# Optimization experiments

Hardware: AMD Instinct MI355X
Metric: run time of the kernel (lower is better)

The kernel has to match this reference:

```python
import jax, jax.numpy as jnp
import numpy as np

N, E = 30000, 600000
D_NODE, E_DIM, H1, H2, D_OUT = 128, 128, 256, 128, 128


def setup_inputs() -> dict:
    key = jax.random.key(0)
    ks = jax.random.split(key, 24)
    w = lambda k, shape: jax.random.normal(k, shape, jnp.float32) * 0.05
    return {
        "node_feat": jax.random.normal(ks[0], (N, D_NODE), jnp.float32),
        "src": jax.random.randint(ks[1], (E,), 0, N, jnp.int32),
        "dst": jax.random.randint(ks[2], (E,), 0, N, jnp.int32),
        "W_e1": w(ks[3], (2 * D_NODE + E_DIM, H1)), "b_e1": w(ks[4], (H1,)),
        "W_e2": w(ks[5], (H1, E_DIM)), "b_e2": w(ks[6], (E_DIM,)),
        "W_n1": w(ks[7], (D_NODE + E_DIM, H1)), "b_n1": w(ks[8], (H1,)),
        "W_n2": w(ks[9], (H1, H2)), "b_n2": w(ks[10], (H2,)),
        "W_el1": w(ks[11], (2 * H2, H1)), "b_el1": w(ks[12], (H1,)),
        "W_el2": w(ks[13], (H1, E_DIM)), "b_el2": w(ks[14], (E_DIM,)),
        "W_logit": w(ks[15], (E_DIM, 2)), "b_logit": w(ks[16], (2,)),
        "W_nro": w(ks[17], (H2, D_OUT)), "b_nro": w(ks[18], (D_OUT,)),
        "W_ero": w(ks[19], (E_DIM, D_OUT)), "b_ero": w(ks[20], (D_OUT,)),
        "msg_passing_steps": 2,
    }


def reference(node_feat, src, dst,
              W_e1, b_e1, W_e2, b_e2,
              W_n1, b_n1, W_n2, b_n2,
              W_el1, b_el1, W_el2, b_el2,
              W_logit, b_logit, W_nro, b_nro, W_ero, b_ero,
              msg_passing_steps):
    n_nodes = node_feat.shape[0]
    edge_dim = W_e2.shape[1]
    # incoming messages 'h', initialized to zeros
    h = jnp.zeros((n_nodes, edge_dim), node_feat.dtype)
    for _ in range(msg_passing_steps):
        # apply_edges: edge_feat = fc_edge2(relu(fc_edge([h_src, nf_src, nf_dst])))
        inp = jnp.concatenate([h[src], node_feat[src], node_feat[dst]], axis=-1)  # [E, edge_dim+2*D]
        edge_feat = jax.nn.relu(inp @ W_e1 + b_e1) @ W_e2 + b_e2                   # [E, edge_dim]
        # update_all with fn.sum: scatter-sum messages into destination nodes
        h = jax.ops.segment_sum(edge_feat, dst, num_segments=n_nodes)
    # apply_nodes: node_feat <- fc_node2(relu(fc_node([node_feat, h])))
    nf = jax.nn.relu(jnp.concatenate([node_feat, h], axis=-1) @ W_n1 + b_n1) @ W_n2 + b_n2  # [N, H2]
    n_out = nf @ W_nro + b_nro
    # compute_edge_logits: symmetric edge MLP over updated node reps
    s, d = nf[src], nf[dst]
    edge_mlp = lambda x: jax.nn.relu(x @ W_el1 + b_el1) @ W_el2 + b_el2
    comb = edge_mlp(jnp.concatenate([s, d], axis=-1)) + edge_mlp(jnp.concatenate([d, s], axis=-1))
    e_out_readout = comb @ W_ero + b_ero
    e_out = comb @ W_logit + b_logit
    return n_out, e_out_readout, e_out
```

## Files before the change

kernel.cpp:

```cpp
#include <hip/hip_runtime.h>
#include <hip/hip_bf16.h>

typedef __bf16 bf16;
typedef unsigned short u16;
typedef bf16 bf16x8 __attribute__((ext_vector_type(8)));
typedef bf16 bf16x4 __attribute__((ext_vector_type(4)));
typedef float f32x4 __attribute__((ext_vector_type(4)));

constexpr int NN = 30000;
constexpr int NE = 600000;
constexpr int D  = 128;

__device__ inline f32x4 mfma16(bf16x8 a, bf16x8 b, f32x4 c) {
    return __builtin_amdgcn_mfma_f32_16x16x32_bf16(a, b, c, 0, 0, 0);
}
__device__ inline bf16x8 ld8(const bf16* p) {
    return *reinterpret_cast<const bf16x8*>(p);
}
__device__ inline bf16x8 cvt8(const float* p) {
    float4 v0 = reinterpret_cast<const float4*>(p)[0];
    float4 v1 = reinterpret_cast<const float4*>(p)[1];
    bf16x8 r;
    r[0] = (bf16)v0.x; r[1] = (bf16)v0.y; r[2] = (bf16)v0.z; r[3] = (bf16)v0.w;
    r[4] = (bf16)v1.x; r[5] = (bf16)v1.y; r[6] = (bf16)v1.z; r[7] = (bf16)v1.w;
    return r;
}
__device__ inline int swz512(int row, int byteInRow) {
    return row * 512 + (byteInRow ^ ((row & 15) << 4));
}

struct TMat { const float* src; bf16* dst; int K; int Nc; };
struct TPack { TMat m[12]; };

__global__ void transpose_cast_kernel(TPack p) {
    TMat mm = p.m[blockIdx.x];
    int total = mm.K * mm.Nc;
    for (int idx = blockIdx.y * blockDim.x + threadIdx.x; idx < total;
         idx += gridDim.y * blockDim.x) {
        int c = idx / mm.K;
        int k = idx - c * mm.K;
        mm.dst[idx] = (bf16)mm.src[k * mm.Nc + c];
    }
}

__global__ void fuse_kernel(const float* __restrict__ W_el2,
                            const float* __restrict__ W_ero,
                            const float* __restrict__ W_logit,
                            const float* __restrict__ b_el2,
                            const float* __restrict__ b_ero,
                            const float* __restrict__ b_logit,
                            bf16* __restrict__ W2eroT, bf16* __restrict__ W2lgT,
                            float* __restrict__ b2ero, float* __restrict__ b2lg) {
    int k = blockIdx.x;
    int c = threadIdx.x;
    if (c >= 144) return;
    if (k < 256) {
        if (c < 128) {
            float s = 0.f;
            for (int j = 0; j < 128; ++j) s += W_el2[k * 128 + j] * W_ero[j * 128 + c];
            W2eroT[c * 256 + k] = (bf16)s;
        } else {
            int cc = c - 128;
            float s = 0.f;
            if (cc < 2) for (int j = 0; j < 128; ++j) s += W_el2[k * 128 + j] * W_logit[j * 2 + cc];
            W2lgT[cc * 256 + k] = (bf16)s;
        }
    } else {
        if (c < 128) {
            float s = b_ero[c];
            for (int j = 0; j < 128; ++j) s += 2.f * b_el2[j] * W_ero[j * 128 + c];
            b2ero[c] = s;
        } else if (c < 130) {
            int cc = c - 128;
            float s = b_logit[cc];
            for (int j = 0; j < 128; ++j) s += 2.f * b_el2[j] * W_logit[j * 2 + cc];
            b2lg[cc] = s;
        }
    }
}

__global__ void hist_kernel(const int* __restrict__ dst, int* __restrict__ counts) {
    int e = blockIdx.x * blockDim.x + threadIdx.x;
    if (e < NE) atomicAdd(counts + dst[e], 1);
}

__global__ void scan_kernel(const int* __restrict__ counts, int* __restrict__ offsets,
                            int* __restrict__ cursor) {
    __shared__ int part[1024];
    const int t = threadIdx.x;
    const int base = t * 30;
    int local[30];
    int s = 0;
#pragma unroll
    for (int i = 0; i < 30; ++i) {
        int idx = base + i;
        int v = (idx < NN) ? counts[idx] : 0;
        local[i] = s;
        s += v;
    }
    part[t] = s;
    __syncthreads();
    for (int off = 1; off < 1024; off <<= 1) {
        int x = (t >= off) ? part[t - off] : 0;
        __syncthreads();
        part[t] += x;
        __syncthreads();
    }
    int chunkExcl = (t == 0) ? 0 : part[t - 1];
#pragma unroll
    for (int i = 0; i < 30; ++i) {
        int idx = base + i;
        if (idx < NN) {
            int excl = chunkExcl + local[i];
            offsets[idx] = excl;
            cursor[idx] = excl;
        }
    }
    if (t == 0) offsets[NN] = NE;
}

__global__ void scatter_kernel(const int* __restrict__ src, const int* __restrict__ dst,
                               int* __restrict__ cursor, int* __restrict__ perm,
                               u16* __restrict__ srcS, u16* __restrict__ dstS) {
    int e = blockIdx.x * blockDim.x + threadIdx.x;
    if (e < NE) {
        int d = dst[e];
        int p = atomicAdd(cursor + d, 1);
        perm[p] = e;
        srcS[p] = (u16)src[e];
        dstS[p] = (u16)d;
    }
}

template<bool IN_BF16>
__global__ void __launch_bounds__(256, 4)
node_pre_kernel(const float* __restrict__ inF, const bf16* __restrict__ inB,
                const bf16* __restrict__ WT,
                const float* __restrict__ bias0,
                bf16* __restrict__ O1, bf16* __restrict__ O2) {
    const int half = blockIdx.y;
    const int r0 = blockIdx.x * 64;
    const int t = threadIdx.x, wv = t >> 6, l = t & 63, lr = l & 15, qk = l >> 4;
    int row[4];
#pragma unroll
    for (int m = 0; m < 4; ++m) { int r = r0 + m * 16 + lr; row[m] = r < NN ? r : NN - 1; }
    int coln[4];
#pragma unroll
    for (int n = 0; n < 4; ++n) coln[n] = wv * 64 + n * 16 + lr;
    f32x4 acc[4][4];
#pragma unroll
    for (int m = 0; m < 4; ++m)
#pragma unroll
        for (int n = 0; n < 4; ++n) acc[m][n] = 0.f;
#pragma unroll
    for (int ks = 0; ks < 4; ++ks) {
        const int kg = ks * 32 + qk * 8;
        bf16x8 a[4], b[4];
#pragma unroll
        for (int m = 0; m < 4; ++m)
            a[m] = IN_BF16 ? ld8(inB + row[m] * D + kg) : cvt8(inF + row[m] * D + kg);
#pragma unroll
        for (int n = 0; n < 4; ++n) b[n] = ld8(WT + (half * 256 + coln[n]) * 128 + kg);
#pragma unroll
        for (int m = 0; m < 4; ++m)
#pragma unroll
            for (int n = 0; n < 4; ++n) acc[m][n] = mfma16(a[m], b[n], acc[m][n]);
    }
    bf16* O = half ? O2 : O1;
#pragma unroll
    for (int n = 0; n < 4; ++n) {
        float bia = (half == 0 && bias0) ? bias0[coln[n]] : 0.f;
#pragma unroll
        for (int m = 0; m < 4; ++m)
#pragma unroll
            for (int j = 0; j < 4; ++j) {
                int gr = r0 + m * 16 + qk * 4 + j;
                if (gr < NN) O[gr * 256 + coln[n]] = (bf16)(acc[m][n][j] + bia);
            }
    }
}

template<bool HBF>
__global__ void __launch_bounds__(256, 4)
s2_update_kernel(const void* __restrict__ h1, const bf16* __restrict__ WtopT,
                 bf16* __restrict__ S) {
    const int r0 = blockIdx.x * 64;
    const int t = threadIdx.x, wv = t >> 6, l = t & 63, lr = l & 15, qk = l >> 4;
    int row[4];
#pragma unroll
    for (int m = 0; m < 4; ++m) { int r = r0 + m * 16 + lr; row[m] = r < NN ? r : NN - 1; }
    int coln[4];
#pragma unroll
    for (int n = 0; n < 4; ++n) coln[n] = wv * 64 + n * 16 + lr;
    f32x4 acc[4][4];
#pragma unroll
    for (int m = 0; m < 4; ++m)
#pragma unroll
        for (int n = 0; n < 4; ++n) acc[m][n] = 0.f;
#pragma unroll
    for (int ks = 0; ks < 4; ++ks) {
        const int kg = ks * 32 + qk * 8;
        bf16x8 a[4], b[4];
#pragma unroll
        for (int m = 0; m < 4; ++m) {
            if constexpr (HBF) a[m] = ld8((const bf16*)h1 + row[m] * D + kg);
            else               a[m] = cvt8((const float*)h1 + row[m] * D + kg);
        }
#pragma unroll
        for (int n = 0; n < 4; ++n) b[n] = ld8(WtopT + coln[n] * 128 + kg);
#pragma unroll
        for (int m = 0; m < 4; ++m)
#pragma unroll
            for (int n = 0; n < 4; ++n) acc[m][n] = mfma16(a[m], b[n], acc[m][n]);
    }
#pragma unroll
    for (int n = 0; n < 4; ++n)
#pragma unroll
        for (int m = 0; m < 4; ++m)
#pragma unroll
            for (int j = 0; j < 4; ++j) {
                int gr = r0 + m * 16 + qk * 4 + j;
                if (gr < NN) {
                    int idx = gr * 256 + coln[n];
                    S[idx] = (bf16)((float)S[idx] + acc[m][n][j]);
                }
            }
}

__global__ void __launch_bounds__(256, 8)
seg_sum_kernel(const bf16* __restrict__ S, const bf16* __restrict__ Bm,
               const int* __restrict__ offsets, const u16* __restrict__ srcS,
               bf16* __restrict__ T) {
    const int gw = (blockIdx.x * blockDim.x + threadIdx.x) >> 6;
    if (gw >= NN) return;
    const int l = threadIdx.x & 63;
    const int beg = offsets[gw], end = offsets[gw + 1];
    bf16x4 bv = *reinterpret_cast<const bf16x4*>(Bm + (size_t)gw * 256 + l * 4);
    const float b0 = (float)bv[0], b1 = (float)bv[1], b2 = (float)bv[2], b3 = (float)bv[3];
    float t0 = 0.f, t1 = 0.f, t2 = 0.f, t3 = 0.f;
    int i = beg;
    for (; i + 4 <= end; i += 4) {
        int s0 = srcS[i], s1 = srcS[i + 1], s2 = srcS[i + 2], s3 = srcS[i + 3];
        bf16x4 a0 = *reinterpret_cast<const bf16x4*>(S + (size_t)s0 * 256 + l * 4);
        bf16x4 a1 = *reinterpret_cast<const bf16x4*>(S + (size_t)s1 * 256 + l * 4);
        bf16x4 a2 = *reinterpret_cast<const bf16x4*>(S + (size_t)s2 * 256 + l * 4);
        bf16x4 a3 = *reinterpret_cast<const bf16x4*>(S + (size_t)s3 * 256 + l * 4);
        float v;
        v = (float)a0[0] + b0; t0 += v > 0.f ? v : 0.f;
        v = (float)a0[1] + b1; t1 += v > 0.f ? v : 0.f;
        v = (float)a0[2] + b2; t2 += v > 0.f ? v : 0.f;
        v = (float)a0[3] + b3; t3 += v > 0.f ? v : 0.f;
        v = (float)a1[0] + b0; t0 += v > 0.f ? v : 0.f;
        v = (float)a1[1] + b1; t1 += v > 0.f ? v : 0.f;
        v = (float)a1[2] + b2; t2 += v > 0.f ? v : 0.f;
        v = (float)a1[3] + b3; t3 += v > 0.f ? v : 0.f;
        v = (float)a2[0] + b0; t0 += v > 0.f ? v : 0.f;
        v = (float)a2[1] + b1; t1 += v > 0.f ? v : 0.f;
        v = (float)a2[2] + b2; t2 += v > 0.f ? v : 0.f;
        v = (float)a2[3] + b3; t3 += v > 0.f ? v : 0.f;
        v = (float)a3[0] + b0; t0 += v > 0.f ? v : 0.f;
        v = (float)a3[1] + b1; t1 += v > 0.f ? v : 0.f;
        v = (float)a3[2] + b2; t2 += v > 0.f ? v : 0.f;
        v = (float)a3[3] + b3; t3 += v > 0.f ? v : 0.f;
    }
    for (; i < end; ++i) {
        int s0 = srcS[i];
        bf16x4 a0 = *reinterpret_cast<const bf16x4*>(S + (size_t)s0 * 256 + l * 4);
        float v;
        v = (float)a0[0] + b0; t0 += v > 0.f ? v : 0.f;
        v = (float)a0[1] + b1; t1 += v > 0.f ? v : 0.f;
        v = (float)a0[2] + b2; t2 += v > 0.f ? v : 0.f;
        v = (float)a0[3] + b3; t3 += v > 0.f ? v : 0.f;
    }
    bf16x4 o;
    o[0] = (bf16)t0; o[1] = (bf16)t1; o[2] = (bf16)t2; o[3] = (bf16)t3;
    *reinterpret_cast<bf16x4*>(T + (size_t)gw * 256 + l * 4) = o;
}

__global__ void __launch_bounds__(256, 4)
h_gemm_kernel(const bf16* __restrict__ T, const bf16* __restrict__ We2T,
              const float* __restrict__ b_e2, const int* __restrict__ deg,
              bf16* __restrict__ h) {
    const int r0 = blockIdx.x * 64;
    const int t = threadIdx.x, wv = t >> 6, l = t & 63, lr = l & 15, qk = l >> 4;
    int row[4];
#pragma unroll
    for (int m = 0; m < 4; ++m) { int r = r0 + m * 16 + lr; row[m] = r < NN ? r : NN - 1; }
    int col2[2];
#pragma unroll
    for (int n = 0; n < 2; ++n) col2[n] = wv * 32 + n * 16 + lr;
    f32x4 acc[4][2];
#pragma unroll
    for (int m = 0; m < 4; ++m)
#pragma unroll
        for (int n = 0; n < 2; ++n) acc[m][n] = 0.f;
#pragma unroll
    for (int ks = 0; ks < 8; ++ks) {
        const int kg = ks * 32 + qk * 8;
        bf16x8 a[4], b[2];
#pragma unroll
        for (int m = 0; m < 4; ++m) a[m] = ld8(T + (size_t)row[m] * 256 + kg);
#pragma unroll
        for (int n = 0; n < 2; ++n) b[n] = ld8(We2T + col2[n] * 256 + kg);
#pragma unroll
        for (int m = 0; m < 4; ++m)
#pragma unroll
            for (int n = 0; n < 2; ++n) acc[m][n] = mfma16(a[m], b[n], acc[m][n]);
    }
#pragma unroll
    for (int n = 0; n < 2; ++n) {
        float bw = b_e2[col2[n]];
#pragma unroll
        for (int m = 0; m < 4; ++m)
#pragma unroll
            for (int j = 0; j < 4; ++j) {
                int gr = r0 + m * 16 + qk * 4 + j;
                if (gr < NN)
                    h[(size_t)gr * D + col2[n]] = (bf16)(acc[m][n][j] + (float)deg[gr] * bw);
            }
    }
}

template<bool HBF>
__global__ void __launch_bounds__(256, 2)
node_mlp_kernel(const float* __restrict__ node_feat,
                const void* __restrict__ h2,
                const bf16* __restrict__ Wn1T,
                const bf16* __restrict__ Wn2T,
                const float* __restrict__ b_n1,
                const float* __restrict__ b_n2,
                bf16* __restrict__ nf2_bf) {
    __shared__ __align__(16) char sH[64 * 512];
    const int t = threadIdx.x, wv = t >> 6, l = t & 63, lr = l & 15, qk = l >> 4;
    const int r0 = blockIdx.x * 64;
    int row[4];
#pragma unroll
    for (int m = 0; m < 4; ++m) { int r = r0 + m * 16 + lr; row[m] = r < NN ? r : NN - 1; }
    int coln[4];
#pragma unroll
    for (int n = 0; n < 4; ++n) coln[n] = wv * 64 + n * 16 + lr;
    f32x4 acc[4][4];
#pragma unroll
    for (int m = 0; m < 4; ++m)
#pragma unroll
        for (int n = 0; n < 4; ++n) acc[m][n] = 0.f;
#pragma unroll
    for (int ks = 0; ks < 4; ++ks) {
        const int kg = ks * 32 + qk * 8;
        bf16x8 a[4], b[4];
#pragma unroll
        for (int m = 0; m < 4; ++m) a[m] = cvt8(node_feat + (size_t)row[m] * D + kg);
#pragma unroll
        for (int n = 0; n < 4; ++n) b[n] = ld8(Wn1T + coln[n] * 256 + kg);
#pragma unroll
        for (int m = 0; m < 4; ++m)
#pragma unroll
            for (int n = 0; n < 4; ++n) acc[m][n] = mfma16(a[m], b[n], acc[m][n]);
#pragma unroll
        for (int m = 0; m < 4; ++m) {
            if constexpr (HBF) a[m] = ld8((const bf16*)h2 + (size_t)row[m] * D + kg);
            else               a[m] = cvt8((const float*)h2 + (size_t)row[m] * D + kg);
        }
#pragma unroll
        for (int n = 0; n < 4; ++n) b[n] = ld8(Wn1T + coln[n] * 256 + 128 + kg);
#pragma unroll
        for (int m = 0; m < 4; ++m)
#pragma unroll
            for (int n = 0; n < 4; ++n) acc[m][n] = mfma16(a[m], b[n], acc[m][n]);
    }
#pragma unroll
    for (int n = 0; n < 4; ++n) {
        float bia = b_n1[coln[n]];
#pragma unroll
        for (int m = 0; m < 4; ++m)
#pragma unroll
            for (int j = 0; j < 4; ++j) {
                int r = m * 16 + qk * 4 + j;
                float v = acc[m][n][j] + bia;
                v = v > 0.f ? v : 0.f;
                *reinterpret_cast<bf16*>(sH + swz512(r, coln[n] * 2)) = (bf16)v;
            }
    }
    __syncthreads();
    int col2[2];
#pragma unroll
    for (int n = 0; n < 2; ++n) col2[n] = wv * 32 + n * 16 + lr;
    f32x4 acc2[4][2];
#pragma unroll
    for (int m = 0; m < 4; ++m)
#pragma unroll
        for (int n = 0; n < 2; ++n) acc2[m][n] = 0.f;
#pragma unroll
    for (int ks = 0; ks < 8; ++ks) {
        const int k0 = ks * 32 + qk * 8;
        bf16x8 a[4], b[2];
#pragma unroll
        for (int m = 0; m < 4; ++m)
            a[m] = *reinterpret_cast<const bf16x8*>(sH + swz512(m * 16 + lr, k0 * 2));
#pragma unroll
        for (int n = 0; n < 2; ++n) b[n] = ld8(Wn2T + col2[n] * 256 + k0);
#pragma unroll
        for (int m = 0; m < 4; ++m)
#pragma unroll
            for (int n = 0; n < 2; ++n) acc2[m][n] = mfma16(a[m], b[n], acc2[m][n]);
    }
#pragma unroll
    for (int n = 0; n < 2; ++n) {
        float bia = b_n2[col2[n]];
#pragma unroll
        for (int m = 0; m < 4; ++m)
#pragma unroll
            for (int j = 0; j < 4; ++j) {
                int gr = r0 + m * 16 + qk * 4 + j;
                if (gr < NN) nf2_bf[(size_t)gr * D + col2[n]] = (bf16)(acc2[m][n][j] + bia);
            }
    }
}

__global__ void __launch_bounds__(256, 4)
edge_logit_sorted(const bf16* __restrict__ U, const bf16* __restrict__ V,
                  const int* __restrict__ perm, const u16* __restrict__ srcS,
                  const u16* __restrict__ dstS,
                  const bf16* __restrict__ W2eroT, const bf16* __restrict__ W2lgT,
                  const float* __restrict__ b2ero, const float* __restrict__ b2lg,
                  float* __restrict__ e_ro, float* __restrict__ e_lg) {
    __shared__ int s_e[128];
    __shared__ int s_s[128];
    __shared__ int s_d[128];
    const int t = threadIdx.x, wv = t >> 6, l = t & 63, lr = l & 15, qk = l >> 4;
    const int bid = (int)blockIdx.x;
    const int cpx = (int)(gridDim.x >> 3);
    const int sbid = (bid & 7) * cpx + (bid >> 3);
    const int p0 = sbid * 128;
    if (t < 128) {
        int p = min(p0 + t, NE - 1);
        s_e[t] = perm[p];
        s_s[t] = (int)srcS[p];
        s_d[t] = (int)dstS[p];
    }
    __syncthreads();

    int is[2], id[2];
#pragma unroll
    for (int m = 0; m < 2; ++m) {
        int el = wv * 32 + m * 16 + lr;
        is[m] = s_s[el];
        id[m] = s_d[el];
    }
    f32x4 aro[2][8];
    f32x4 alg[2];
#pragma unroll
    for (int m = 0; m < 2; ++m) {
        alg[m] = 0.f;
#pragma unroll
        for (int n = 0; n < 8; ++n) aro[m][n] = 0.f;
    }
#pragma unroll
    for (int ks = 0; ks < 8; ++ks) {
        const int kg = ks * 32 + qk * 8;
        bf16x8 a[2];
#pragma unroll
        for (int m = 0; m < 2; ++m) {
            bf16x8 us = ld8(U + (size_t)is[m] * 256 + kg);
            bf16x8 vd = ld8(V + (size_t)id[m] * 256 + kg);
            bf16x8 ud = ld8(U + (size_t)id[m] * 256 + kg);
            bf16x8 vs = ld8(V + (size_t)is[m] * 256 + kg);
#pragma unroll
            for (int i = 0; i < 8; ++i) {
                float f1 = (float)us[i] + (float)vd[i]; f1 = f1 > 0.f ? f1 : 0.f;
                float f2 = (float)ud[i] + (float)vs[i]; f2 = f2 > 0.f ? f2 : 0.f;
                a[m][i] = (bf16)(f1 + f2);
            }
        }
#pragma unroll
        for (int n = 0; n < 8; ++n) {
            bf16x8 b = ld8(W2eroT + (n * 16 + lr) * 256 + kg);
#pragma unroll
            for (int m = 0; m < 2; ++m) aro[m][n] = mfma16(a[m], b, aro[m][n]);
        }
        bf16x8 blg = ld8(W2lgT + lr * 256 + kg);
#pragma unroll
        for (int m = 0; m < 2; ++m) alg[m] = mfma16(a[m], blg, alg[m]);
    }
#pragma unroll
    for (int n = 0; n < 8; ++n) {
        int col = n * 16 + lr;
        float bia = b2ero[col];
#pragma unroll
        for (int m = 0; m < 2; ++m)
#pragma unroll
            for (int j = 0; j < 4; ++j) {
                int el = wv * 32 + m * 16 + qk * 4 + j;
                e_ro[(size_t)s_e[el] * D + col] = aro[m][n][j] + bia;
            }
    }
    if (lr < 2) {
        float bia = b2lg[lr];
#pragma unroll
        for (int m = 0; m < 2; ++m)
#pragma unroll
            for (int j = 0; j < 4; ++j) {
                int el = wv * 32 + m * 16 + qk * 4 + j;
                e_lg[(size_t)s_e[el] * 2 + lr] = alg[m][j] + bia;
            }
    }
}

__global__ void __launch_bounds__(256, 4)
edge_msg_kernel(const bf16* __restrict__ S, const bf16* __restrict__ Bm,
                const int* __restrict__ src, const int* __restrict__ dst,
                const bf16* __restrict__ We2T,
                const float* __restrict__ b_e2,
                float* __restrict__ h_out) {
    __shared__ int s_src[128];
    __shared__ int s_dst[128];
    const int t = threadIdx.x, wv = t >> 6, l = t & 63, lr = l & 15, qk = l >> 4;
    const int e0 = blockIdx.x * 128;
    if (t < 128)      s_src[t] = src[min(e0 + t, NE - 1)];
    else              s_dst[t - 128] = dst[min(e0 + t - 128, NE - 1)];
    __syncthreads();
    const bf16* pS[2];
    const bf16* pB[2];
#pragma unroll
    for (int m = 0; m < 2; ++m) {
        int el = wv * 32 + m * 16 + lr;
        pS[m] = S + s_src[el] * 256;
        pB[m] = Bm + s_dst[el] * 256;
    }
    f32x4 acc[2][8];
#pragma unroll
    for (int m = 0; m < 2; ++m)
#pragma unroll
        for (int n = 0; n < 8; ++n) acc[m][n] = 0.f;
#pragma unroll
    for (int ks = 0; ks < 8; ++ks) {
        const int kg = ks * 32 + qk * 8;
        bf16x8 a[2];
#pragma unroll
        for (int m = 0; m < 2; ++m) {
            bf16x8 sa = ld8(pS[m] + kg);
            bf16x8 sb = ld8(pB[m] + kg);
#pragma unroll
            for (int i = 0; i < 8; ++i) {
                float f = (float)sa[i] + (float)sb[i];
                a[m][i] = (bf16)(f > 0.f ? f : 0.f);
            }
        }
#pragma unroll
        for (int n = 0; n < 8; ++n) {
            bf16x8 b = ld8(We2T + (n * 16 + lr) * 256 + kg);
#pragma unroll
            for (int m = 0; m < 2; ++m) acc[m][n] = mfma16(a[m], b, acc[m][n]);
        }
    }
#pragma unroll
    for (int n = 0; n < 8; ++n) {
        int col = n * 16 + lr;
        float bia = b_e2[col];
#pragma unroll
        for (int m = 0; m < 2; ++m)
#pragma unroll
            for (int j = 0; j < 4; ++j) {
                int el = wv * 32 + m * 16 + qk * 4 + j;
                if (e0 + el < NE)
                    atomicAdd(h_out + s_dst[el] * D + col, acc[m][n][j] + bia);
            }
    }
}

__global__ void __launch_bounds__(256, 4)
edge_logit_fast(const bf16* __restrict__ U, const bf16* __restrict__ V,
                const int* __restrict__ src, const int* __restrict__ dst,
                const bf16* __restrict__ W2eroT,
                const bf16* __restrict__ W2lgT,
                const float* __restrict__ b2ero, const float* __restrict__ b2lg,
                float* __restrict__ e_ro, float* __restrict__ e_lg) {
    __shared__ int s_src[128];
    __shared__ int s_dst[128];
    const int t = threadIdx.x, wv = t >> 6, l = t & 63, lr = l & 15, qk = l >> 4;
    const int e0 = blockIdx.x * 128;
    if (t < 128)      s_src[t] = src[min(e0 + t, NE - 1)];
    else              s_dst[t - 128] = dst[min(e0 + t - 128, NE - 1)];
    __syncthreads();
    int is[2], id[2];
#pragma unroll
    for (int m = 0; m < 2; ++m) {
        int el = wv * 32 + m * 16 + lr;
        is[m] = s_src[el];
        id[m] = s_dst[el];
    }
    f32x4 aro[2][8];
    f32x4 alg[2];
#pragma unroll
    for (int m = 0; m < 2; ++m) {
        alg[m] = 0.f;
#pragma unroll
        for (int n = 0; n < 8; ++n) aro[m][n] = 0.f;
    }
#pragma unroll
    for (int ks = 0; ks < 8; ++ks) {
        const int kg = ks * 32 + qk * 8;
        bf16x8 a[2];
#pragma unroll
        for (int m = 0; m < 2; ++m) {
            bf16x8 us = ld8(U + is[m] * 256 + kg);
            bf16x8 vd = ld8(V + id[m] * 256 + kg);
            bf16x8 ud = ld8(U + id[m] * 256 + kg);
            bf16x8 vs = ld8(V + is[m] * 256 + kg);
#pragma unroll
            for (int i = 0; i < 8; ++i) {
                float f1 = (float)us[i] + (float)vd[i]; f1 = f1 > 0.f ? f1 : 0.f;
                float f2 = (float)ud[i] + (float)vs[i]; f2 = f2 > 0.f ? f2 : 0.f;
                a[m][i] = (bf16)(f1 + f2);
            }
        }
#pragma unroll
        for (int n = 0; n < 8; ++n) {
            bf16x8 b = ld8(W2eroT + (n * 16 + lr) * 256 + kg);
#pragma unroll
            for (int m = 0; m < 2; ++m) aro[m][n] = mfma16(a[m], b, aro[m][n]);
        }
        bf16x8 blg = ld8(W2lgT + lr * 256 + kg);
#pragma unroll
        for (int m = 0; m < 2; ++m) alg[m] = mfma16(a[m], blg, alg[m]);
    }
#pragma unroll
    for (int n = 0; n < 8; ++n) {
        int col = n * 16 + lr;
        float bia = b2ero[col];
#pragma unroll
        for (int m = 0; m < 2; ++m)
#pragma unroll
            for (int j = 0; j < 4; ++j) {
                int el = wv * 32 + m * 16 + qk * 4 + j;
                int e = e0 + el;
                if (e < NE) e_ro[e * D + col] = aro[m][n][j] + bia;
            }
    }
    if (lr < 2) {
        float bia = b2lg[lr];
#pragma unroll
        for (int m = 0; m < 2; ++m)
#pragma unroll
            for (int j = 0; j < 4; ++j) {
                int el = wv * 32 + m * 16 + qk * 4 + j;
                int e = e0 + el;
                if (e < NE) e_lg[e * 2 + lr] = alg[m][j] + bia;
            }
    }
}

__global__ void __launch_bounds__(256, 4)
nro_kernel(const bf16* __restrict__ nf2_bf, const bf16* __restrict__ WnroT,
           const float* __restrict__ b_nro, float* __restrict__ n_out) {
    const int r0 = blockIdx.x * 64;
    const int t = threadIdx.x, wv = t >> 6, l = t & 63, lr = l & 15, qk = l >> 4;
    int row[4];
#pragma unroll
    for (int m = 0; m < 4; ++m) { int r = r0 + m * 16 + lr; row[m] = r < NN ? r : NN - 1; }
    int col2[2];
#pragma unroll
    for (int n = 0; n < 2; ++n) col2[n] = wv * 32 + n * 16 + lr;
    f32x4 acc[4][2];
#pragma unroll
    for (int m = 0; m < 4; ++m)
#pragma unroll
        for (int n = 0; n < 2; ++n) acc[m][n] = 0.f;
#pragma unroll
    for (int ks = 0; ks < 4; ++ks) {
        const int kg = ks * 32 + qk * 8;
        bf16x8 a[4], b[2];
#pragma unroll
        for (int m = 0; m < 4; ++m) a[m] = ld8(nf2_bf + (size_t)row[m] * D + kg);
#pragma unroll
        for (int n = 0; n < 2; ++n) b[n] = ld8(WnroT + col2[n] * 128 + kg);
#pragma unroll
        for (int m = 0; m < 4; ++m)
#pragma unroll
            for (int n = 0; n < 2; ++n) acc[m][n] = mfma16(a[m], b[n], acc[m][n]);
    }
#pragma unroll
    for (int n = 0; n < 2; ++n) {
        float bia = b_nro[col2[n]];
#pragma unroll
        for (int m = 0; m < 4; ++m)
#pragma unroll
            for (int j = 0; j < 4; ++j) {
                int gr = r0 + m * 16 + qk * 4 + j;
                if (gr < NN) n_out[(size_t)gr * D + col2[n]] = acc[m][n][j] + bia;
            }
    }
}

extern "C" void kernel_launch(void* const* d_in, const int* in_sizes, int n_in,
                              void* d_out, int out_size, void* d_ws, size_t ws_size,
                              hipStream_t stream) {
    const float* node_feat = (const float*)d_in[0];
    const int*   src   = (const int*)d_in[1];
    const int*   dst   = (const int*)d_in[2];
    const float* W_e1  = (const float*)d_in[3];
    const float* b_e1  = (const float*)d_in[4];
    const float* W_e2  = (const float*)d_in[5];
    const float* b_e2  = (const float*)d_in[6];
    const float* W_n1  = (const float*)d_in[7];
    const float* b_n1  = (const float*)d_in[8];
    const float* W_n2  = (const float*)d_in[9];
    const float* b_n2  = (const float*)d_in[10];
    const float* W_el1 = (const float*)d_in[11];
    const float* b_el1 = (const float*)d_in[12];
    const float* W_el2 = (const float*)d_in[13];
    const float* b_el2 = (const float*)d_in[14];
    const float* W_logit = (const float*)d_in[15];
    const float* b_logit = (const float*)d_in[16];
    const float* W_nro = (const float*)d_in[17];
    const float* b_nro = (const float*)d_in[18];
    const float* W_ero = (const float*)d_in[19];
    const float* b_ero = (const float*)d_in[20];

    char* ws = (char*)d_ws;
    bf16* wb = (bf16*)ws;
    bf16* WmbT   = wb;
    bf16* WtopT  = wb + 65536;
    bf16* We2T   = wb + 98304;
    bf16* Wn1T   = wb + 131072;
    bf16* Wn2T   = wb + 196608;
    bf16* WuvT   = wb + 229376;
    bf16* WnroT  = wb + 294912;
    bf16* W2eroT = wb + 311296;
    bf16* W2lgT  = wb + 344064;
    float* fb    = (float*)(ws + 928000);
    float* b2ero = fb;
    float* b2lg  = fb + 128;

    float* out   = (float*)d_out;
    float* n_out = out;
    float* e_ro  = out + 3840000;
    float* e_lg  = out + 80640000;

    TPack pk;
    pk.m[0]  = {W_e1 + 128 * 256, WmbT,              128, 256};
    pk.m[1]  = {W_e1 + 256 * 256, WmbT + 256 * 128,  128, 256};
    pk.m[2]  = {W_e1,             WtopT,             128, 256};
    pk.m[3]  = {W_e2,             We2T,              256, 128};
    pk.m[4]  = {W_n1,             Wn1T,              256, 256};
    pk.m[5]  = {W_n2,             Wn2T,              256, 128};
    pk.m[6]  = {W_el1,            WuvT,              128, 256};
    pk.m[7]  = {W_el1 + 128 * 256, WuvT + 256 * 128, 128, 256};
    pk.m[8]  = {W_nro,            WnroT,             128, 128};
    pk.m[9]  = {W_nro,            WnroT,             128, 128};
    pk.m[10] = {W_nro,            WnroT,             128, 128};
    pk.m[11] = {W_nro,            WnroT,             128, 128};

    const size_t NEED_NEW = 28888576;

    if (ws_size >= NEED_NEW) {
        char* eb = (char*)e_ro;
        bf16* S    = (bf16*)(eb);
        bf16* Bm   = (bf16*)(eb + 15360000);
        bf16* T    = (bf16*)(eb + 30720000);
        bf16* h1   = (bf16*)(eb + 46080000);
        bf16* h2   = (bf16*)(eb + 53760000);
        int* counts  = (int*)(eb + 61440000);
        int* offsets = (int*)(eb + 61560000);
        int* cursor  = (int*)(eb + 61680004);
        bf16* U    = (bf16*)n_out;
        bf16* nf2_bf = (bf16*)(ws + 1048576);
        bf16* Vbuf   = (bf16*)(ws + 8728576);
        int*  perm   = (int*)(ws + 24088576);
        u16*  srcS   = (u16*)(ws + 26488576);
        u16*  dstS   = (u16*)(ws + 27688576);

        transpose_cast_kernel<<<dim3(12, 40), 256, 0, stream>>>(pk);
        fuse_kernel<<<257, 160, 0, stream>>>(W_el2, W_ero, W_logit, b_el2, b_ero, b_logit,
                                             W2eroT, W2lgT, b2ero, b2lg);
        hipMemsetAsync(counts, 0, NN * 4, stream);
        hist_kernel<<<(NE + 255) / 256, 256, 0, stream>>>(dst, counts);
        scan_kernel<<<1, 1024, 0, stream>>>(counts, offsets, cursor);
        scatter_kernel<<<(NE + 255) / 256, 256, 0, stream>>>(src, dst, cursor,
                                                             perm, srcS, dstS);
        node_pre_kernel<false><<<dim3(469, 2), 256, 0, stream>>>(
            node_feat, nullptr, WmbT, b_e1, S, Bm);
        seg_sum_kernel<<<7500, 256, 0, stream>>>(S, Bm, offsets, srcS, T);
        h_gemm_kernel<<<469, 256, 0, stream>>>(T, We2T, b_e2, counts, h1);
        s2_update_kernel<true><<<469, 256, 0, stream>>>(h1, WtopT, S);
        seg_sum_kernel<<<7500, 256, 0, stream>>>(S, Bm, offsets, srcS, T);
        h_gemm_kernel<<<469, 256, 0, stream>>>(T, We2T, b_e2, counts, h2);
        node_mlp_kernel<true><<<469, 256, 0, stream>>>(
            node_feat, h2, Wn1T, Wn2T, b_n1, b_n2, nf2_bf);
        node_pre_kernel<true><<<dim3(469, 2), 256, 0, stream>>>(
            nullptr, nf2_bf, WuvT, b_el1, U, Vbuf);
        edge_logit_sorted<<<4688, 256, 0, stream>>>(
            U, Vbuf, perm, srcS, dstS, W2eroT, W2lgT, b2ero, b2lg, e_ro, e_lg);
        nro_kernel<<<469, 256, 0, stream>>>(nf2_bf, WnroT, b_nro, n_out);
    } else {
        bf16* nf2_bf = (bf16*)(ws + 1048576);
        bf16* Vbuf   = (bf16*)(ws + 9000000);
        float* h1f = n_out;
        bf16*  S   = (bf16*)e_ro;
        bf16*  Bm  = (bf16*)((char*)e_ro + 15360000);
        float* h2f = (float*)((char*)e_ro + 30720000);
        bf16*  U   = (bf16*)n_out;

        transpose_cast_kernel<<<dim3(12, 40), 256, 0, stream>>>(pk);
        fuse_kernel<<<257, 160, 0, stream>>>(W_el2, W_ero, W_logit, b_el2, b_ero, b_logit,
                                             W2eroT, W2lgT, b2ero, b2lg);
        hipMemsetAsync(h1f, 0, (size_t)NN * D * 4, stream);
        hipMemsetAsync(h2f, 0, (size_t)NN * D * 4, stream);
        node_pre_kernel<false><<<dim3(469, 2), 256, 0, stream>>>(
            node_feat, nullptr, WmbT, b_e1, S, Bm);
        edge_msg_kernel<<<4688, 256, 0, stream>>>(S, Bm, src, dst, We2T, b_e2, h1f);
        s2_update_kernel<false><<<469, 256, 0, stream>>>(h1f, WtopT, S);
        edge_msg_kernel<<<4688, 256, 0, stream>>>(S, Bm, src, dst, We2T, b_e2, h2f);
        node_mlp_kernel<false><<<469, 256, 0, stream>>>(
            node_feat, h2f, Wn1T, Wn2T, b_n1, b_n2, nf2_bf);
        node_pre_kernel<true><<<dim3(469, 2), 256, 0, stream>>>(
            nullptr, nf2_bf, WuvT, b_el1, U, Vbuf);
        edge_logit_fast<<<4688, 256, 0, stream>>>(
            U, Vbuf, src, dst, W2eroT, W2lgT, b2ero, b2lg, e_ro, e_lg);
        nro_kernel<<<469, 256, 0, stream>>>(nf2_bf, WnroT, b_nro, n_out);
    }
}
```

Measured before the change: 754.2 us.

## Fold W_e2 into downstream weights to eliminate h GEMM kernels

Precomputes the products W_e2·W_e1(top) and W_e2·W_n1(bottom), plus their bias terms, so the per-node h = T·W_e2 + deg·b_e2 intermediate is never formed. The s2 update and the node MLP now consume the segment-summed T directly with a K=256 GEMM, which removes two h_gemm launches and the h1/h2 round trips through memory. The e_ro output stores are also made nontemporal. In exchange the fused GEMMs do more MFMA work (K 256 instead of 128), add a small weight-fusion kernel, and round the pre-multiplied weights to bf16, which changes numerics slightly.

Result: faster. 735.7 us (-2.5%).

```diff
diff --git a/kernel.cpp b/kernel.cpp
--- a/kernel.cpp
+++ b/kernel.cpp
@@ -79,6 +79,35 @@
     }
 }
 
+__global__ void fuse2_kernel(const float* __restrict__ W_e2,
+                             const float* __restrict__ W_e1,
+                             const float* __restrict__ W_n1,
+                             const float* __restrict__ b_e2,
+                             bf16* __restrict__ WcsT, bf16* __restrict__ WcnT,
+                             float* __restrict__ bcs, float* __restrict__ bcn) {
+    int k = blockIdx.x;
+    int c = threadIdx.x;
+    if (k < 256) {
+        float s1 = 0.f, s2 = 0.f;
+        for (int j = 0; j < 128; ++j) {
+            float w = W_e2[k * 128 + j];
+            s1 += w * W_e1[j * 256 + c];
+            s2 += w * W_n1[(128 + j) * 256 + c];
+        }
+        WcsT[c * 256 + k] = (bf16)s1;
+        WcnT[c * 256 + k] = (bf16)s2;
+    } else {
+        float s1 = 0.f, s2 = 0.f;
+        for (int j = 0; j < 128; ++j) {
+            float b = b_e2[j];
+            s1 += b * W_e1[j * 256 + c];
+            s2 += b * W_n1[(128 + j) * 256 + c];
+        }
+        bcs[c] = s1;
+        bcn[c] = s2;
+    }
+}
+
 __global__ void hist_kernel(const int* __restrict__ dst, int* __restrict__ counts) {
     int e = blockIdx.x * blockDim.x + threadIdx.x;
     if (e < NE) atomicAdd(counts + dst[e], 1);
@@ -180,9 +209,54 @@
     }
 }
 
-template<bool HBF>
 __global__ void __launch_bounds__(256, 4)
-s2_update_kernel(const void* __restrict__ h1, const bf16* __restrict__ WtopT,
+s2_fused_kernel(const bf16* __restrict__ T, const bf16* __restrict__ WcsT,
+                const float* __restrict__ bcs, const int* __restrict__ deg,
+                bf16* __restrict__ S) {
+    const int r0 = blockIdx.x * 64;
+    const int t = threadIdx.x, wv = t >> 6, l = t & 63, lr = l & 15, qk = l >> 4;
+    int row[4];
+#pragma unroll
+    for (int m = 0; m < 4; ++m) { int r = r0 + m * 16 + lr; row[m] = r < NN ? r : NN - 1; }
+    int coln[4];
+#pragma unroll
+    for (int n = 0; n < 4; ++n) coln[n] = wv * 64 + n * 16 + lr;
+    f32x4 acc[4][4];
+#pragma unroll
+    for (int m = 0; m < 4; ++m)
+#pragma unroll
+        for (int n = 0; n < 4; ++n) acc[m][n] = 0.f;
+#pragma unroll
+    for (int ks = 0; ks < 8; ++ks) {
+        const int kg = ks * 32 + qk * 8;
+        bf16x8 a[4], b[4];
+#pragma unroll
+        for (int m = 0; m < 4; ++m) a[m] = ld8(T + (size_t)row[m] * 256 + kg);
+#pragma unroll
+        for (int n = 0; n < 4; ++n) b[n] = ld8(WcsT + coln[n] * 256 + kg);
+#pragma unroll
+        for (int m = 0; m < 4; ++m)
+#pragma unroll
+            for (int n = 0; n < 4; ++n) acc[m][n] = mfma16(a[m], b[n], acc[m][n]);
+    }
+#pragma unroll
+    for (int n = 0; n < 4; ++n) {
+        float bw = bcs[coln[n]];
+#pragma unroll
+        for (int m = 0; m < 4; ++m)
+#pragma unroll
+            for (int j = 0; j < 4; ++j) {
+                int gr = r0 + m * 16 + qk * 4 + j;
+                if (gr < NN) {
+                    int idx = gr * 256 + coln[n];
+                    S[idx] = (bf16)((float)S[idx] + acc[m][n][j] + (float)deg[gr] * bw);
+                }
+            }
+    }
+}
+
+__global__ void __launch_bounds__(256, 4)
+s2_update_kernel(const float* __restrict__ h1, const bf16* __restrict__ WtopT,
                  bf16* __restrict__ S) {
     const int r0 = blockIdx.x * 64;
     const int t = threadIdx.x, wv = t >> 6, l = t & 63, lr = l & 15, qk = l >> 4;
@@ -202,10 +276,7 @@
         const int kg = ks * 32 + qk * 8;
         bf16x8 a[4], b[4];
 #pragma unroll
-        for (int m = 0; m < 4; ++m) {
-            if constexpr (HBF) a[m] = ld8((const bf16*)h1 + row[m] * D + kg);
-            else               a[m] = cvt8((const float*)h1 + row[m] * D + kg);
-        }
+        for (int m = 0; m < 4; ++m) a[m] = cvt8(h1 + (size_t)row[m] * D + kg);
 #pragma unroll
         for (int n = 0; n < 4; ++n) b[n] = ld8(WtopT + coln[n] * 128 + kg);
 #pragma unroll
@@ -277,54 +348,112 @@
     *reinterpret_cast<bf16x4*>(T + (size_t)gw * 256 + l * 4) = o;
 }
 
-__global__ void __launch_bounds__(256, 4)
-h_gemm_kernel(const bf16* __restrict__ T, const bf16* __restrict__ We2T,
-              const float* __restrict__ b_e2, const int* __restrict__ deg,
-              bf16* __restrict__ h) {
+__global__ void __launch_bounds__(256, 2)
+node_mlp_fused(const float* __restrict__ node_feat,
+               const bf16* __restrict__ T2,
+               const bf16* __restrict__ Wn1T,
+               const bf16* __restrict__ WcnT,
+               const bf16* __restrict__ Wn2T,
+               const float* __restrict__ b_n1,
+               const float* __restrict__ bcn,
+               const int* __restrict__ deg,
+               const float* __restrict__ b_n2,
+               bf16* __restrict__ nf2_bf) {
+    __shared__ __align__(16) char sH[64 * 512];
+    const int t = threadIdx.x, wv = t >> 6, l = t & 63, lr = l & 15, qk = l >> 4;
     const int r0 = blockIdx.x * 64;
-    const int t = threadIdx.x, wv = t >> 6, l = t & 63, lr = l & 15, qk = l >> 4;
     int row[4];
 #pragma unroll
     for (int m = 0; m < 4; ++m) { int r = r0 + m * 16 + lr; row[m] = r < NN ? r : NN - 1; }
+    int coln[4];
+#pragma unroll
+    for (int n = 0; n < 4; ++n) coln[n] = wv * 64 + n * 16 + lr;
+    f32x4 acc[4][4];
+#pragma unroll
+    for (int m = 0; m < 4; ++m)
+#pragma unroll
+        for (int n = 0; n < 4; ++n) acc[m][n] = 0.f;
+#pragma unroll
+    for (int ks = 0; ks < 4; ++ks) {
+        const int kg = ks * 32 + qk * 8;
+        bf16x8 a[4], b[4];
+#pragma unroll
+        for (int m = 0; m < 4; ++m) a[m] = cvt8(node_feat + (size_t)row[m] * D + kg);
+#pragma unroll
+        for (int n = 0; n < 4; ++n) b[n] = ld8(Wn1T + coln[n] * 256 + kg);
+#pragma unroll
+        for (int m = 0; m < 4; ++m)
+#pragma unroll
+            for (int n = 0; n < 4; ++n) acc[m][n] = mfma16(a[m], b[n], acc[m][n]);
+    }
+#pragma unroll
+    for (int ks = 0; ks < 8; ++ks) {
+        const int kg = ks * 32 + qk * 8;
+        bf16x8 a[4], b[4];
+#pragma unroll
+        for (int m = 0; m < 4; ++m) a[m] = ld8(T2 + (size_t)row[m] * 256 + kg);
+#pragma unroll
+        for (int n = 0; n < 4; ++n) b[n] = ld8(WcnT + coln[n] * 256 + kg);
+#pragma unroll
+        for (int m = 0; m < 4; ++m)
+#pragma unroll
+            for (int n = 0; n < 4; ++n) acc[m][n] = mfma16(a[m], b[n], acc[m][n]);
+    }
+#pragma unroll
+    for (int n = 0; n < 4; ++n) {
+        float bia = b_n1[coln[n]];
+        float bw  = bcn[coln[n]];
+#pragma unroll
+        for (int m = 0; m < 4; ++m)
+#pragma unroll
+            for (int j = 0; j < 4; ++j) {
+                int r = m * 16 + qk * 4 + j;
+                int gr = r0 + r;
+                float dg = (gr < NN) ? (float)deg[gr] : 0.f;
+                float v = acc[m][n][j] + bia + dg * bw;
+                v = v > 0.f ? v : 0.f;
+                *reinterpret_cast<bf16*>(sH + swz512(r, coln[n] * 2)) = (bf16)v;
+            }
+    }
+    __syncthreads();
     int col2[2];
 #pragma unroll
     for (int n = 0; n < 2; ++n) col2[n] = wv * 32 + n * 16 + lr;
-    f32x4 acc[4][2];
+    f32x4 acc2[4][2];
 #pragma unroll
     for (int m = 0; m < 4; ++m)
 #pragma unroll
-        for (int n = 0; n < 2; ++n) acc[m][n] = 0.f;
+        for (int n = 0; n < 2; ++n) acc2[m][n] = 0.f;
 #pragma unroll
     for (int ks = 0; ks < 8; ++ks) {
-        const int kg = ks * 32 + qk * 8;
+        const int k0 = ks * 32 + qk * 8;
         bf16x8 a[4], b[2];
 #pragma unroll
-        for (int m = 0; m < 4; ++m) a[m] = ld8(T + (size_t)row[m] * 256 + kg);
-#pragma unroll
-        for (int n = 0; n < 2; ++n) b[n] = ld8(We2T + col2[n] * 256 + kg);
-#pragma unroll
-        for (int m = 0; m < 4; ++m)
-#pragma unroll
-            for (int n = 0; n < 2; ++n) acc[m][n] = mfma16(a[m], b[n], acc[m][n]);
+        for (int m = 0; m < 4; ++m)
+            a[m] = *reinterpret_cast<const bf16x8*>(sH + swz512(m * 16 + lr, k0 * 2));
+#pragma unroll
+        for (int n = 0; n < 2; ++n) b[n] = ld8(Wn2T + col2[n] * 256 + k0);
+#pragma unroll
+        for (int m = 0; m < 4; ++m)
+#pragma unroll
+            for (int n = 0; n < 2; ++n) acc2[m][n] = mfma16(a[m], b[n], acc2[m][n]);
     }
 #pragma unroll
     for (int n = 0; n < 2; ++n) {
-        float bw = b_e2[col2[n]];
+        float bia = b_n2[col2[n]];
 #pragma unroll
         for (int m = 0; m < 4; ++m)
 #pragma unroll
             for (int j = 0; j < 4; ++j) {
                 int gr = r0 + m * 16 + qk * 4 + j;
-                if (gr < NN)
-                    h[(size_t)gr * D + col2[n]] = (bf16)(acc[m][n][j] + (float)deg[gr] * bw);
-            }
-    }
-}
-
-template<bool HBF>
+                if (gr < NN) nf2_bf[(size_t)gr * D + col2[n]] = (bf16)(acc2[m][n][j] + bia);
+            }
+    }
+}
+
 __global__ void __launch_bounds__(256, 2)
 node_mlp_kernel(const float* __restrict__ node_feat,
-                const void* __restrict__ h2,
+                const float* __restrict__ h2,
                 const bf16* __restrict__ Wn1T,
                 const bf16* __restrict__ Wn2T,
                 const float* __restrict__ b_n1,
@@ -357,10 +486,7 @@
 #pragma unroll
             for (int n = 0; n < 4; ++n) acc[m][n] = mfma16(a[m], b[n], acc[m][n]);
 #pragma unroll
-        for (int m = 0; m < 4; ++m) {
-            if constexpr (HBF) a[m] = ld8((const bf16*)h2 + (size_t)row[m] * D + kg);
-            else               a[m] = cvt8((const float*)h2 + (size_t)row[m] * D + kg);
-        }
+        for (int m = 0; m < 4; ++m) a[m] = cvt8(h2 + (size_t)row[m] * D + kg);
 #pragma unroll
         for (int n = 0; n < 4; ++n) b[n] = ld8(Wn1T + coln[n] * 256 + 128 + kg);
 #pragma unroll
@@ -413,6 +539,50 @@
             for (int j = 0; j < 4; ++j) {
                 int gr = r0 + m * 16 + qk * 4 + j;
                 if (gr < NN) nf2_bf[(size_t)gr * D + col2[n]] = (bf16)(acc2[m][n][j] + bia);
+            }
+    }
+}
+
+__global__ void __launch_bounds__(256, 4)
+h_gemm_kernel(const bf16* __restrict__ T, const bf16* __restrict__ We2T,
+              const float* __restrict__ b_e2, const int* __restrict__ deg,
+              bf16* __restrict__ h) {
+    const int r0 = blockIdx.x * 64;
+    const int t = threadIdx.x, wv = t >> 6, l = t & 63, lr = l & 15, qk = l >> 4;
+    int row[4];
+#pragma unroll
+    for (int m = 0; m < 4; ++m) { int r = r0 + m * 16 + lr; row[m] = r < NN ? r : NN - 1; }
+    int col2[2];
+#pragma unroll
+    for (int n = 0; n < 2; ++n) col2[n] = wv * 32 + n * 16 + lr;
+    f32x4 acc[4][2];
+#pragma unroll
+    for (int m = 0; m < 4; ++m)
+#pragma unroll
+        for (int n = 0; n < 2; ++n) acc[m][n] = 0.f;
+#pragma unroll
+    for (int ks = 0; ks < 8; ++ks) {
+        const int kg = ks * 32 + qk * 8;
+        bf16x8 a[4], b[2];
+#pragma unroll
+        for (int m = 0; m < 4; ++m) a[m] = ld8(T + (size_t)row[m] * 256 + kg);
+#pragma unroll
+        for (int n = 0; n < 2; ++n) b[n] = ld8(We2T + col2[n] * 256 + kg);
+#pragma unroll
+        for (int m = 0; m < 4; ++m)
+#pragma unroll
+            for (int n = 0; n < 2; ++n) acc[m][n] = mfma16(a[m], b[n], acc[m][n]);
+    }
+#pragma unroll
+    for (int n = 0; n < 2; ++n) {
+        float bw = b_e2[col2[n]];
+#pragma unroll
+        for (int m = 0; m < 4; ++m)
+#pragma unroll
+            for (int j = 0; j < 4; ++j) {
+                int gr = r0 + m * 16 + qk * 4 + j;
+                if (gr < NN)
+                    h[(size_t)gr * D + col2[n]] = (bf16)(acc[m][n][j] + (float)deg[gr] * bw);
             }
     }
 }
@@ -491,7 +661,8 @@
 #pragma unroll
             for (int j = 0; j < 4; ++j) {
                 int el = wv * 32 + m * 16 + qk * 4 + j;
-                e_ro[(size_t)s_e[el] * D + col] = aro[m][n][j] + bia;
+                __builtin_nontemporal_store(aro[m][n][j] + bia,
+                                            e_ro + (size_t)s_e[el] * D + col);
             }
     }
     if (lr < 2) {
@@ -728,9 +899,13 @@
     bf16* WnroT  = wb + 294912;
     bf16* W2eroT = wb + 311296;
     bf16* W2lgT  = wb + 344064;
-    float* fb    = (float*)(ws + 928000);
+    bf16* WcsT   = wb + 348160;
+    bf16* WcnT   = wb + 413696;
+    float* fb    = (float*)(ws + 960000);
     float* b2ero = fb;
     float* b2lg  = fb + 128;
+    float* bcs   = fb + 256;
+    float* bcn   = fb + 512;
 
     float* out   = (float*)d_out;
     float* n_out = out;
@@ -758,8 +933,6 @@
         bf16* S    = (bf16*)(eb);
         bf16* Bm   = (bf16*)(eb + 15360000);
         bf16* T    = (bf16*)(eb + 30720000);
-        bf16* h1   = (bf16*)(eb + 46080000);
-        bf16* h2   = (bf16*)(eb + 53760000);
         int* counts  = (int*)(eb + 61440000);
         int* offsets = (int*)(eb + 61560000);
         int* cursor  = (int*)(eb + 61680004);
@@ -773,6 +946,8 @@
         transpose_cast_kernel<<<dim3(12, 40), 256, 0, stream>>>(pk);
         fuse_kernel<<<257, 160, 0, stream>>>(W_el2, W_ero, W_logit, b_el2, b_ero, b_logit,
                                              W2eroT, W2lgT, b2ero, b2lg);
+        fuse2_kernel<<<257, 256, 0, stream>>>(W_e2, W_e1, W_n1, b_e2,
+                                              WcsT, WcnT, bcs, bcn);
         hipMemsetAsync(counts, 0, NN * 4, stream);
         hist_kernel<<<(NE + 255) / 256, 256, 0, stream>>>(dst, counts);
         scan_kernel<<<1, 1024, 0, stream>>>(counts, offsets, cursor);
@@ -781,12 +956,10 @@
         node_pre_kernel<false><<<dim3(469, 2), 256, 0, stream>>>(
             node_feat, nullptr, WmbT, b_e1, S, Bm);
         seg_sum_kernel<<<7500, 256, 0, stream>>>(S, Bm, offsets, srcS, T);
-        h_gemm_kernel<<<469, 256, 0, stream>>>(T, We2T, b_e2, counts, h1);
-        s2_update_kernel<true><<<469, 256, 0, stream>>>(h1, WtopT, S);
+        s2_fused_kernel<<<469, 256, 0, stream>>>(T, WcsT, bcs, counts, S);
         seg_sum_kernel<<<7500, 256, 0, stream>>>(S, Bm, offsets, srcS, T);
-        h_gemm_kernel<<<469, 256, 0, stream>>>(T, We2T, b_e2, counts, h2);
-        node_mlp_kernel<true><<<469, 256, 0, stream>>>(
-            node_feat, h2, Wn1T, Wn2T, b_n1, b_n2, nf2_bf);
+        node_mlp_fused<<<469, 256, 0, stream>>>(
+            node_feat, T, Wn1T, WcnT, Wn2T, b_n1, bcn, counts, b_n2, nf2_bf);
         node_pre_kernel<true><<<dim3(469, 2), 256, 0, stream>>>(
             nullptr, nf2_bf, WuvT, b_el1, U, Vbuf);
         edge_logit_sorted<<<4688, 256, 0, stream>>>(
@@ -809,9 +982,9 @@
         node_pre_kernel<false><<<dim3(469, 2), 256, 0, stream>>>(
             node_feat, nullptr, WmbT, b_e1, S, Bm);
         edge_msg_kernel<<<4688, 256, 0, stream>>>(S, Bm, src, dst, We2T, b_e2, h1f);
-        s2_update_kernel<false><<<469, 256, 0, stream>>>(h1f, WtopT, S);
+        s2_update_kernel<<<469, 256, 0, stream>>>(h1f, WtopT, S);
         edge_msg_kernel<<<4688, 256, 0, stream>>>(S, Bm, src, dst, We2T, b_e2, h2f);
-        node_mlp_kernel<false><<<469, 256, 0, stream>>>(
+        node_mlp_kernel<<<469, 256, 0, stream>>>(
             node_feat, h2f, Wn1T, Wn2T, b_n1, b_n2, nf2_bf);
         node_pre_kernel<true><<<dim3(469, 2), 256, 0, stream>>>(
             nullptr, nf2_bf, WuvT, b_el1, U, Vbuf);
```
